# Kernel tuning notes

Measured on AMD Instinct MI355X. Metric: run time of the kernel, lower is better.

Reference implementation:

```python
import jax, jax.numpy as jnp
import numpy as np


def setup_inputs() -> dict:
    key = jax.random.key(0)
    k1, k2 = jax.random.split(key)
    N, M, D = 8192, 8192, 128
    z_anc = jax.random.normal(k1, (N, D), dtype=jnp.float32)
    z_pos_neg = jax.random.normal(k2, (M, D), dtype=jnp.float32)
    return {"z_anc": z_anc, "z_pos_neg": z_pos_neg}


def reference(z_anc, z_pos_neg):
    # -||a_i - b_j||_2 computed via the GEMM expansion
    # ||a-b||^2 = ||a||^2 + ||b||^2 - 2 a.b  (avoids the O(N*M*D) broadcast)
    a2 = jnp.sum(z_anc * z_anc, axis=-1)          # [N]
    b2 = jnp.sum(z_pos_neg * z_pos_neg, axis=-1)  # [M]
    ab = jnp.einsum("nd,md->nm", z_anc, z_pos_neg)  # [N, M]
    d2 = jnp.maximum(a2[:, None] + b2[None, :] - 2.0 * ab, 0.0)
    return -jnp.sqrt(d2)
```

## Files before the change

kernel.cpp:

```cpp
#include <hip/hip_runtime.h>
#include <hip/hip_bf16.h>

#define D_DIM 128
#define TILE 128
#define LDS_K (D_DIM + 8)

typedef __attribute__((ext_vector_type(8))) short short8;
typedef __attribute__((ext_vector_type(4))) float floatx4;

__global__ void prep_kernel(const float* __restrict__ za, const float* __restrict__ zb,
                            __hip_bfloat16* __restrict__ abf, __hip_bfloat16* __restrict__ bbf,
                            float* __restrict__ a2, float* __restrict__ b2, int N) {
    int r = blockIdx.x * 4 + (threadIdx.x >> 6);
    int lane = threadIdx.x & 63;
    const float* src; __hip_bfloat16* dst; float* nrm; int row;
    if (r < N) { src = za; dst = abf; nrm = a2; row = r; }
    else       { src = zb; dst = bbf; nrm = b2; row = r - N; }
    const float2 v = ((const float2*)(src + (size_t)row * D_DIM))[lane];
    __hip_bfloat16 h0 = __float2bfloat16(v.x);
    __hip_bfloat16 h1 = __float2bfloat16(v.y);
    float f0 = __bfloat162float(h0), f1 = __bfloat162float(h1);
    float ss = f0 * f0 + f1 * f1;
    ushort2 st;
    st.x = *(const unsigned short*)&h0;
    st.y = *(const unsigned short*)&h1;
    ((ushort2*)(dst + (size_t)row * D_DIM))[lane] = st;
    #pragma unroll
    for (int off = 32; off; off >>= 1) ss += __shfl_down(ss, off, 64);
    if (lane == 0) nrm[row] = ss;
}

__global__ __launch_bounds__(256, 2)
void dist_kernel(const __hip_bfloat16* __restrict__ abf, const __hip_bfloat16* __restrict__ bbf,
                 const float* __restrict__ a2, const float* __restrict__ b2,
                 float* __restrict__ out, int M) {
    __shared__ __hip_bfloat16 As[TILE][LDS_K];
    __shared__ __hip_bfloat16 Bs[TILE][LDS_K];

    const int rowBase = blockIdx.y * TILE;
    const int colBase = blockIdx.x * TILE;
    const int tid = threadIdx.x;

    #pragma unroll
    for (int pass = 0; pass < 8; ++pass) {
        int idx = pass * 256 + tid;
        int row = idx >> 4;
        int kc  = (idx & 15) * 8;
        uint4 va = *(const uint4*)(abf + ((size_t)(rowBase + row) * D_DIM + kc));
        *(uint4*)(&As[row][kc]) = va;
        uint4 vb = *(const uint4*)(bbf + ((size_t)(colBase + row) * D_DIM + kc));
        *(uint4*)(&Bs[row][kc]) = vb;
    }
    __syncthreads();

    const int wave = tid >> 6;
    const int lane = tid & 63;
    const int wr = (wave >> 1) * 64;
    const int wc = (wave & 1) * 64;
    const int lrow = lane & 15;
    const int lk = (lane >> 4) * 8;

    floatx4 acc[4][4] = {};
    #pragma unroll
    for (int ks = 0; ks < 4; ++ks) {
        const int k0 = ks * 32 + lk;
        short8 afr[4], bfr[4];
        #pragma unroll
        for (int i = 0; i < 4; ++i)
            afr[i] = *(const short8*)(&As[wr + i * 16 + lrow][k0]);
        #pragma unroll
        for (int j = 0; j < 4; ++j)
            bfr[j] = *(const short8*)(&Bs[wc + j * 16 + lrow][k0]);
        #pragma unroll
        for (int i = 0; i < 4; ++i)
            #pragma unroll
            for (int j = 0; j < 4; ++j)
                acc[i][j] = __builtin_amdgcn_mfma_f32_16x16x32_bf16(afr[i], bfr[j], acc[i][j], 0, 0, 0);
    }

    const int crow0 = rowBase + wr + (lane >> 4) * 4;
    const int ccol0 = colBase + wc + lrow;
    #pragma unroll
    for (int i = 0; i < 4; ++i) {
        #pragma unroll
        for (int r = 0; r < 4; ++r) {
            const int n = crow0 + i * 16 + r;
            const float an = a2[n];
            const size_t rowOff = (size_t)n * (size_t)M;
            #pragma unroll
            for (int j = 0; j < 4; ++j) {
                const int m = ccol0 + j * 16;
                float d2 = an + b2[m] - 2.0f * acc[i][j][r];
                d2 = fmaxf(d2, 0.0f);
                out[rowOff + m] = -sqrtf(d2);
            }
        }
    }
}

extern "C" void kernel_launch(void* const* d_in, const int* in_sizes, int n_in,
                              void* d_out, int out_size, void* d_ws, size_t ws_size,
                              hipStream_t stream) {
    const float* za = (const float*)d_in[0];
    const float* zb = (const float*)d_in[1];
    const int N = in_sizes[0] / D_DIM;
    const int M = in_sizes[1] / D_DIM;
    float* out = (float*)d_out;

    char* ws = (char*)d_ws;
    __hip_bfloat16* abf = (__hip_bfloat16*)ws;
    __hip_bfloat16* bbf = (__hip_bfloat16*)(ws + (size_t)N * D_DIM * sizeof(__hip_bfloat16));
    float* a2 = (float*)(ws + (size_t)(N + M) * D_DIM * sizeof(__hip_bfloat16));
    float* b2 = a2 + N;

    prep_kernel<<<(N + M) / 4, 256, 0, stream>>>(za, zb, abf, bbf, a2, b2, N);

    dim3 grid(M / TILE, N / TILE);
    dist_kernel<<<grid, 256, 0, stream>>>(abf, bbf, a2, b2, out, M);
}
```

Baseline: 277.0 us.

## Drop LDS staging, load MFMA fragments from global, vectorize output stores

Removes the shared-memory tiles and barrier, so each wave loads its bf16 fragments straight from global memory (relying on L1/L2 for reuse). It swaps the MFMA operand roles so each lane holds four consecutive output columns, which allows 16-byte float4 stores of the output and vector loads of b2. Occupancy hint raised from 2 to 3 blocks per CU. The cost is redundant global and cache traffic for operands that were shared through LDS before.

```diff
diff --git a/kernel.cpp b/kernel.cpp
--- a/kernel.cpp
+++ b/kernel.cpp
@@ -3,7 +3,6 @@
 
 #define D_DIM 128
 #define TILE 128
-#define LDS_K (D_DIM + 8)
 
 typedef __attribute__((ext_vector_type(8))) short short8;
 typedef __attribute__((ext_vector_type(4))) float floatx4;
@@ -30,70 +29,68 @@
     if (lane == 0) nrm[row] = ss;
 }
 
-__global__ __launch_bounds__(256, 2)
+__global__ __launch_bounds__(256, 3)
 void dist_kernel(const __hip_bfloat16* __restrict__ abf, const __hip_bfloat16* __restrict__ bbf,
                  const float* __restrict__ a2, const float* __restrict__ b2,
                  float* __restrict__ out, int M) {
-    __shared__ __hip_bfloat16 As[TILE][LDS_K];
-    __shared__ __hip_bfloat16 Bs[TILE][LDS_K];
-
     const int rowBase = blockIdx.y * TILE;
     const int colBase = blockIdx.x * TILE;
-    const int tid = threadIdx.x;
-
-    #pragma unroll
-    for (int pass = 0; pass < 8; ++pass) {
-        int idx = pass * 256 + tid;
-        int row = idx >> 4;
-        int kc  = (idx & 15) * 8;
-        uint4 va = *(const uint4*)(abf + ((size_t)(rowBase + row) * D_DIM + kc));
-        *(uint4*)(&As[row][kc]) = va;
-        uint4 vb = *(const uint4*)(bbf + ((size_t)(colBase + row) * D_DIM + kc));
-        *(uint4*)(&Bs[row][kc]) = vb;
-    }
-    __syncthreads();
-
+    const int tid  = threadIdx.x;
     const int wave = tid >> 6;
     const int lane = tid & 63;
-    const int wr = (wave >> 1) * 64;
-    const int wc = (wave & 1) * 64;
+    const int wn = (wave >> 1) * 64;
+    const int wm = (wave & 1) * 64;
     const int lrow = lane & 15;
-    const int lk = (lane >> 4) * 8;
+    const int lk8  = (lane >> 4) * 8;
+
+    int aOff[4], bOff[4];
+    #pragma unroll
+    for (int j = 0; j < 4; ++j) {
+        aOff[j] = (rowBase + wn + j * 16 + lrow) * D_DIM;
+        bOff[j] = (colBase + wm + j * 16 + lrow) * D_DIM;
+    }
 
     floatx4 acc[4][4] = {};
     #pragma unroll
     for (int ks = 0; ks < 4; ++ks) {
-        const int k0 = ks * 32 + lk;
+        const int k0 = ks * 32 + lk8;
         short8 afr[4], bfr[4];
         #pragma unroll
-        for (int i = 0; i < 4; ++i)
-            afr[i] = *(const short8*)(&As[wr + i * 16 + lrow][k0]);
+        for (int jm = 0; jm < 4; ++jm)
+            afr[jm] = *(const short8*)(bbf + (bOff[jm] + k0));
         #pragma unroll
-        for (int j = 0; j < 4; ++j)
-            bfr[j] = *(const short8*)(&Bs[wc + j * 16 + lrow][k0]);
+        for (int jn = 0; jn < 4; ++jn)
+            bfr[jn] = *(const short8*)(abf + (aOff[jn] + k0));
         #pragma unroll
-        for (int i = 0; i < 4; ++i)
+        for (int jm = 0; jm < 4; ++jm)
             #pragma unroll
-            for (int j = 0; j < 4; ++j)
-                acc[i][j] = __builtin_amdgcn_mfma_f32_16x16x32_bf16(afr[i], bfr[j], acc[i][j], 0, 0, 0);
+            for (int jn = 0; jn < 4; ++jn)
+                acc[jm][jn] = __builtin_amdgcn_mfma_f32_16x16x32_bf16(afr[jm], bfr[jn], acc[jm][jn], 0, 0, 0);
     }
 
-    const int crow0 = rowBase + wr + (lane >> 4) * 4;
-    const int ccol0 = colBase + wc + lrow;
+    const int mq = (lane >> 4) * 4;
+    float an[4];
+    size_t rowOff[4];
     #pragma unroll
-    for (int i = 0; i < 4; ++i) {
+    for (int jn = 0; jn < 4; ++jn) {
+        const int n = rowBase + wn + jn * 16 + lrow;
+        an[jn] = a2[n];
+        rowOff[jn] = (size_t)n * (size_t)M;
+    }
+    #pragma unroll
+    for (int jm = 0; jm < 4; ++jm) {
+        const int m0 = colBase + wm + jm * 16 + mq;
+        const floatx4 bq = *(const floatx4*)(b2 + m0);
         #pragma unroll
-        for (int r = 0; r < 4; ++r) {
-            const int n = crow0 + i * 16 + r;
-            const float an = a2[n];
-            const size_t rowOff = (size_t)n * (size_t)M;
+        for (int jn = 0; jn < 4; ++jn) {
+            floatx4 v;
             #pragma unroll
-            for (int j = 0; j < 4; ++j) {
-                const int m = ccol0 + j * 16;
-                float d2 = an + b2[m] - 2.0f * acc[i][j][r];
+            for (int r = 0; r < 4; ++r) {
+                float d2 = an[jn] + bq[r] - 2.0f * acc[jm][jn][r];
                 d2 = fmaxf(d2, 0.0f);
-                out[rowOff + m] = -sqrtf(d2);
+                v[r] = -sqrtf(d2);
             }
+            *(floatx4*)(out + rowOff[jn] + m0) = v;
         }
     }
 }
```

New measurement: 349.9 us. 26.3% more time.
